# Performance work log

Hardware: AMD Instinct MI355X
Metric: run time of the kernel (lower is better)

Reference implementation:

```python
import jax, jax.numpy as jnp
import numpy as np

C = 256        # channels per FPN level (in_channels == representation_size)
PATCH = 5      # GNN kernel_size == stride
NEG_SLOPE = 0.2
K = 7          # node_connectivities[0]


def _conv1x1(x, w, b):
    return jnp.einsum('bchw,oc->bohw', x, w) + b[None, :, None, None]


def _conv3x3(x, w, b):
    y = jax.lax.conv_general_dilated(x, w, (1, 1), 'SAME',
                                     dimension_numbers=('NCHW', 'OIHW', 'NCHW'))
    return y + b[None, :, None, None]


def _nearest(x, hout, wout):
    hin, win = x.shape[-2:]
    ih = (jnp.arange(hout) * hin) // hout
    iw = (jnp.arange(wout) * win) // wout
    return x[..., ih, :][..., iw]


def _topk_edges(score, k, n):
    # torch: A.scatter(1, topk_idx, topk_val); edge = nonzero(triu(A)); edge=[col,row]
    vals, idx = jax.lax.top_k(score, k)          # per-row top-k
    row = jnp.repeat(jnp.arange(n), k)
    col = idx.reshape(-1)
    val = vals.reshape(-1)
    # triu keeps col>=row; GATv2Conv removes self loops then re-adds one per node
    mask = (col > row) & (val != 0.0)
    loop = jnp.arange(n)
    src = jnp.concatenate([col, loop])           # PyG edge_index[0] = source
    dst = jnp.concatenate([row, loop])
    emask = jnp.concatenate([mask, jnp.ones((n,), bool)])
    return src, dst, emask


def _gatv2(x, src, dst, emask, wl, bl, wr, br, att, bias, n):
    heads, dout = att.shape
    xl = (x @ wl + bl).reshape(n, heads, dout)   # source transform (lin_l)
    xr = (x @ wr + br).reshape(n, heads, dout)   # target transform (lin_r)
    m = xl[src] + xr[dst]                        # [E, H, D]
    e = jnp.sum(jax.nn.leaky_relu(m, NEG_SLOPE) * att[None], axis=-1)  # [E, H]
    e = jnp.where(emask[:, None], e, -1e30)
    emax = jax.ops.segment_max(e, dst, num_segments=n)
    w = jnp.exp(e - emax[dst]) * emask[:, None]
    denom = jax.ops.segment_sum(w, dst, num_segments=n)
    alpha = w / (denom[dst] + 1e-16)
    out = jax.ops.segment_sum(alpha[..., None] * xl[src], dst, num_segments=n)
    return out.reshape(n, heads * dout) + bias


def _gnn(x, p, k):
    # x: [1, C, H, W], H,W divisible by PATCH
    _, c, hh, ww = x.shape
    nh, nw = hh // PATCH, ww // PATCH
    n = nh * nw
    patches = x[0].reshape(c, nh, PATCH, nw, PATCH).transpose(1, 3, 0, 2, 4)
    patches = patches.reshape(n, c, PATCH, PATCH)
    emb = jax.nn.relu(jnp.einsum('ncij,ocij->no', patches, p['conv1_w']) + p['conv1_b'])
    emb = jax.nn.relu(emb @ p['fc2_w'].T + p['fc2_b'])
    # feature-similarity kNN graph
    src, dst, em = _topk_edges(emb @ emb.T, k, n)
    h = jax.nn.elu(_gatv2(emb, src, dst, em, *p['g1'], n))
    h = jax.nn.elu(_gatv2(h, src, dst, em, *p['g2'], n))
    # spatial kNN graph (k smallest distances; self distance 0 drops out via val!=0)
    ii, jj = jnp.meshgrid(jnp.arange(nh) * PATCH, jnp.arange(nw) * PATCH, indexing='ij')
    centers = jnp.stack([ii.reshape(-1), jj.reshape(-1)], -1).astype(x.dtype)
    dist = jnp.sqrt(jnp.sum((centers[:, None] - centers[None]) ** 2, -1))
    src2, dst2, em2 = _topk_edges(-dist, k, n)
    h2 = jax.nn.elu(_gatv2(emb, src2, dst2, em2, *p['g3'], n))
    h2 = jax.nn.elu(_gatv2(h2, src2, dst2, em2, *p['g4'], n))
    hc = jax.nn.relu(jnp.concatenate([h, h2], 1) @ p['fc3_w'].T + p['fc3_b']) + h2
    # torch: reshape(dim,dim,C).swapdims(-1,0) -> [C, nw, nh]
    grid = jnp.transpose(hc.reshape(nh, nw, c), (2, 1, 0))
    # ConvTranspose2d(C, C, 5, stride=5): non-overlapping tiling
    up = jnp.einsum('cij,coab->oiajb', grid, p['convT_w'])
    up = up.reshape(c, nw * PATCH, nh * PATCH) + p['convT_b'][:, None, None]
    return jax.nn.relu(up)[None]


def _forward(feat0, feat1, inner_w, inner_b, layer_w, layer_b, convT_w, convT_b,
             conv1_w, conv1_b, fc2_w, fc2_b, fc3_w, fc3_b,
             g1_wl, g1_bl, g1_wr, g1_br, g1_att, g1_bias,
             g2_wl, g2_bl, g2_wr, g2_br, g2_att, g2_bias,
             g3_wl, g3_bl, g3_wr, g3_br, g3_att, g3_bias,
             g4_wl, g4_bl, g4_wr, g4_br, g4_att, g4_bias, k):
    feats = [feat0, feat1]
    xs = []
    for i, f in enumerate(feats):
        p = dict(conv1_w=conv1_w[i], conv1_b=conv1_b[i],
                 fc2_w=fc2_w[i], fc2_b=fc2_b[i],
                 fc3_w=fc3_w[i], fc3_b=fc3_b[i],
                 convT_w=convT_w[i], convT_b=convT_b[i],
                 g1=(g1_wl[i], g1_bl[i], g1_wr[i], g1_br[i], g1_att[i], g1_bias[i]),
                 g2=(g2_wl[i], g2_bl[i], g2_wr[i], g2_br[i], g2_att[i], g2_bias[i]),
                 g3=(g3_wl[i], g3_bl[i], g3_wr[i], g3_br[i], g3_att[i], g3_bias[i]),
                 g4=(g4_wl[i], g4_bl[i], g4_wr[i], g4_br[i], g4_att[i], g4_bias[i]))
        xs.append(f + _gnn(f, p, k))
    # top-down FPN
    last = _conv1x1(xs[1], inner_w[1], inner_b[1])
    out1 = _conv3x3(last, layer_w[1], layer_b[1])
    inner0 = _conv1x1(xs[0], inner_w[0], inner_b[0])
    td = _nearest(last, xs[0].shape[-2], xs[0].shape[-1])
    out0 = _conv3x3(inner0 + td, layer_w[0], layer_b[0])
    return out0, out1


def setup_inputs() -> dict:
    key = jax.random.key(0)
    keys = jax.random.split(key, 48)
    it = iter(range(48))
    def rn(shape, s=0.05):
        return (jax.random.normal(keys[next(it)], shape) * s).astype(jnp.float32)
    H8 = 8 * C
    inp = dict(
        feat0=rn((1, C, 200, 200), 1.0),
        feat1=rn((1, C, 100, 100), 1.0),
        inner_w=rn((2, C, C)), inner_b=rn((2, C)),
        layer_w=rn((2, C, C, 3, 3)), layer_b=rn((2, C)),
        convT_w=rn((2, C, C, PATCH, PATCH)), convT_b=rn((2, C)),
        conv1_w=rn((2, C, C, PATCH, PATCH)), conv1_b=rn((2, C)),
        fc2_w=rn((2, C, C)), fc2_b=rn((2, C)),
        fc3_w=rn((2, C, 2 * C)), fc3_b=rn((2, C)),
        g1_wl=rn((2, C, H8)), g1_bl=rn((2, H8)), g1_wr=rn((2, C, H8)), g1_br=rn((2, H8)),
        g1_att=rn((2, 8, C)), g1_bias=rn((2, H8)),
        g2_wl=rn((2, H8, C)), g2_bl=rn((2, C)), g2_wr=rn((2, H8, C)), g2_br=rn((2, C)),
        g2_att=rn((2, 1, C)), g2_bias=rn((2, C)),
        g3_wl=rn((2, C, H8)), g3_bl=rn((2, H8)), g3_wr=rn((2, C, H8)), g3_br=rn((2, H8)),
        g3_att=rn((2, 8, C)), g3_bias=rn((2, H8)),
        g4_wl=rn((2, H8, C)), g4_bl=rn((2, C)), g4_wr=rn((2, H8, C)), g4_br=rn((2, C)),
        g4_att=rn((2, 1, C)), g4_bias=rn((2, C)),
        k=K,
    )
    return inp


def reference(feat0, feat1, inner_w, inner_b, layer_w, layer_b, convT_w, convT_b,
              conv1_w, conv1_b, fc2_w, fc2_b, fc3_w, fc3_b,
              g1_wl, g1_bl, g1_wr, g1_br, g1_att, g1_bias,
              g2_wl, g2_bl, g2_wr, g2_br, g2_att, g2_bias,
              g3_wl, g3_bl, g3_wr, g3_br, g3_att, g3_bias,
              g4_wl, g4_bl, g4_wr, g4_br, g4_att, g4_bias, k):
    return _forward(feat0, feat1, inner_w, inner_b, layer_w, layer_b, convT_w, convT_b,
                    conv1_w, conv1_b, fc2_w, fc2_b, fc3_w, fc3_b,
                    g1_wl, g1_bl, g1_wr, g1_br, g1_att, g1_bias,
                    g2_wl, g2_bl, g2_wr, g2_br, g2_att, g2_bias,
                    g3_wl, g3_bl, g3_wr, g3_br, g3_att, g3_bias,
                    g4_wl, g4_bl, g4_wr, g4_br, g4_att, g4_bias, k)
```

## Files before the change

### kernel.cpp

```cpp
#include <hip/hip_runtime.h>
#include <cstdint>
#include <cstddef>
#include <math.h>

#define KNN 7

using short8  = __attribute__((ext_vector_type(8))) short;
using floatx4 = __attribute__((ext_vector_type(4))) float;

static const size_t OFF_ARENA = 0;
static const size_t OFF_XS0   = 10240000;
static const size_t OFF_XS1   = 20480000;
static const size_t OFF_LAST  = 23040000;
static const size_t OFF_EMB   = 25600000;
static const size_t OFF_EMB2  = 26009600;
static const size_t OFF_XL    = 26419200;
static const size_t OFF_H1    = 32972800;
static const size_t OFF_XL2   = 36249600;
static const size_t OFF_CAT   = 37068800;
static const size_t OFF_HC    = 37888000;
static const size_t OFF_SRCF  = 38400000;
static const size_t OFF_SRCS  = 38411200;
static const size_t OFF_BF_A  = 38422400;
static const size_t OFF_BF_W  = 40122400;
// ... 77 lines not shown
            if (ACT == 1) v = fmaxf(v, 0.f);
            C[(size_t)mm * N + nc] = v;
        }
    }
}

template<int ACT, bool BIAS>
static inline void gemm32(hipStream_t s, const float* A, const float* B, const float* bias,
                          float* C, int M, int N, int K)
{
    dim3 g((N + 63) / 64, (M + 63) / 64);
    gemm_k<ACT, BIAS><<<g, dim3(256), 0, s>>>(A, B, bias, C, M, N, K);
}

enum { BT_NT = 0, BT_CONV2 = 2 };

template<int BT, int ACT, int BAX, bool ADDMAT>
__global__ __launch_bounds__(256)
void bgemm_k(const unsigned short* __restrict__ A, const unsigned short* __restrict__ B,
             const float* __restrict__ bias, const float* __restrict__ bias2, int nsplit,
             const float* __restrict__ Dmat, int Dld,
             float* __restrict__ C, int M, int N, int K, int imH, int imW)
{
    __shared__ unsigned short As[3][4096];
    __shared__ unsigned short Bs[3][4096];
    const int tid  = threadIdx.x;
    const int lane = tid & 63;
    const int wid  = tid >> 6;
    const int quad = lane >> 4;
    const int l15  = lane & 15;
    const int wy = wid >> 1, wx = wid & 1;

    int bxx = blockIdx.x, byy = blockIdx.y;
    if (gridDim.y == 2) {
        const int nbx = gridDim.x;
        const int nwg = nbx * 2;
        const int hw  = byy * nbx + bxx;
        const int q = nwg >> 3, r = nwg & 7;
        const int x8 = hw & 7, d = hw >> 3;
        const int lg = (x8 < r) ? x8 * (q + 1) + d : r * (q + 1) + (x8 - r) * q + d;
        byy = lg & 1; bxx = lg >> 1;
    }
    const int bm0 = byy * 128;
    const int bn0 = bxx * 128;

    floatx4 zero = {0.f, 0.f, 0.f, 0.f};
    floatx4 acc[4][4];
    #pragma unroll
    for (int i = 0; i < 4; i++)
        #pragma unroll
        for (int j = 0; j < 4; j++) acc[i][j] = zero;

    const int l4 = lane >> 2;
    const int swc = (((lane & 3) ^ ((lane >> 3) & 3)) << 3);
    const int r0 = wid * 32 + l4;
    const int r1 = r0 + 16;
    int am0 = bm0 + r0; if (am0 > M - 1) am0 = M - 1;
    int am1 = bm0 + r1; if (am1 > M - 1) am1 = M - 1;
    const unsigned short* aP0 = A + (size_t)am0 * K + swc;
    const unsigned short* aP1 = A + (size_t)am1 * K + swc;

    const unsigned short* bP0;
    const unsigned short* bP1;
    if (BT == BT_NT) {
        int bn0r = bn0 + r0; if (bn0r > N - 1) bn0r = N - 1;
        int bn1r = bn0 + r1; if (bn1r > N - 1) bn1r = N - 1;
        bP0 = B + (size_t)bn0r * K + swc;
        bP1 = B + (size_t)bn1r * K + swc;
    } else {
        const int W2 = imW + 2;
        int pp0 = bn0 + r0; if (pp0 > N - 1) pp0 = N - 1;
        int pp1 = bn0 + r1; if (pp1 > N - 1) pp1 = N - 1;
        const int py0 = pp0 / imW, px0 = pp0 - py0 * imW;
        const int py1 = pp1 / imW, px1 = pp1 - py1 * imW;
        bP0 = B + ((size_t)(py0 + 1) * W2 + px0 + 1) * 256 + swc;
        bP1 = B + ((size_t)(py1 + 1) * W2 + px1 + 1) * 256 + swc;
    }

    auto stage = [&](int buf, int t) {
        const int k0 = t << 5;
        glds16(aP0 + k0, &As[buf][wid * 1024]);
        glds16(aP1 + k0, &As[buf][wid * 1024 + 512]);
        if (BT == BT_NT) {
            glds16(bP0 + k0, &Bs[buf][wid * 1024]);
            glds16(bP1 + k0, &Bs[buf][wid * 1024 + 512]);
        } else {
            const int jj = k0 >> 8;
            const int j3 = jj / 3;
            const ptrdiff_t toff = (ptrdiff_t)((j3 - 1) * (imW + 2) + (jj - j3 * 3 - 1)) * 256
                                 + (k0 & 255);
            glds16(bP0 + toff, &Bs[buf][wid * 1024]);
            glds16(bP1 + toff, &Bs[buf][wid * 1024 + 512]);
        }
    };
    const int rsw = ((quad ^ ((l15 >> 1) & 3)) << 3);
    auto compute = [&](int buf) {
        short8 af[4], bfr[4];
        #pragma unroll
        for (int i = 0; i < 4; i++)
            af[i] = *(const short8*)&As[buf][(wy * 64 + i * 16 + l15) * 32 + rsw];
        #pragma unroll
        for (int j = 0; j < 4; j++)
            bfr[j] = *(const short8*)&Bs[buf][(wx * 64 + j * 16 + l15) * 32 + rsw];
        #pragma unroll
        for (int i = 0; i < 4; i++)
            #pragma unroll
            for (int j = 0; j < 4; j++)
                acc[i][j] = __builtin_amdgcn_mfma_f32_16x16x32_bf16(af[i], bfr[j], acc[i][j], 0, 0, 0);
    };

    const int T = K >> 5;
    stage(0, 0);
    if (T > 1) stage(1, 1);
    int cb = 0, sb = 2;
    for (int t = 0; t < T; t++) {
        if (t < T - 1) asm volatile("s_waitcnt vmcnt(4) lgkmcnt(0)" ::: "memory");
        else           asm volatile("s_waitcnt vmcnt(0) lgkmcnt(0)" ::: "memory");
        __builtin_amdgcn_s_barrier();
        __builtin_amdgcn_sched_barrier(0);
        if (t + 2 < T) stage(sb, t + 2);
        compute(cb);
        cb = (cb == 2) ? 0 : cb + 1;
        sb = (sb == 2) ? 0 : sb + 1;
    }

    #pragma unroll
    for (int i = 0; i < 4; i++) {
        #pragma unroll
        for (int r = 0; r < 4; r++) {
            const int m = bm0 + wy * 64 + i * 16 + quad * 4 + r;
            if (m >= M) continue;
            #pragma unroll
            for (int j = 0; j < 4; j++) {
                const int n = bn0 + wx * 64 + j * 16 + l15;
                if (n >= N) continue;
                float v = acc[i][j][r];
                if (bias != nullptr)
                    v += (BAX == 0) ? bias[m] : (n < nsplit ? bias[n] : bias2[n - nsplit]);
                if (ACT == 1) v = fmaxf(v, 0.f);
                if (ADDMAT) v += Dmat[(size_t)m * Dld + n];
                C[(size_t)m * N + n] = v;
            }
        }
    }
}

template<int BT, int ACT, int BAX, bool ADDMAT>
static inline void bgemm(hipStream_t s, const unsigned short* A, const unsigned short* B,
                         const float* bias, const float* bias2, int nsplit,
                         const float* D, int Dld, float* C,
                         int M, int N, int K, int imH = 0, int imW = 0)
{
    dim3 g((N + 127) / 128, (M + 127) / 128);
    bgemm_k<BT, ACT, BAX, ADDMAT><<<g, dim3(256), 0, s>>>(A, B, bias, bias2, nsplit,
                                                          D, Dld, C, M, N, K, imH, imW);
}

__global__ __launch_bounds__(256)
void bgemm_sk_k(const unsigned short* __restrict__ A, const unsigned short* __restrict__ B,
                float* __restrict__ part, int M, int N, int K, int Kc)
{
    __shared__ unsigned short As[3][4096];
    __shared__ unsigned short Bs[3][4096];
    const int tid  = threadIdx.x;
    const int lane = tid & 63;
    const int wid  = tid >> 6;
    const int quad = lane >> 4;
    const int l15  = lane & 15;
    const int wy = wid >> 1, wx = wid & 1;
    const int bm0 = blockIdx.y * 128;
    const int bn0 = blockIdx.x * 128;
    const int kbeg = blockIdx.z * Kc;
    const int kend = (kbeg + Kc < K) ? kbeg + Kc : K;

    floatx4 zero = {0.f, 0.f, 0.f, 0.f};
    floatx4 acc[4][4];
    #pragma unroll
    for (int i = 0; i < 4; i++)
        #pragma unroll
        for (int j = 0; j < 4; j++) acc[i][j] = zero;

    const int l4 = lane >> 2;
    const int swc = (((lane & 3) ^ ((lane >> 3) & 3)) << 3);
    const int r0 = wid * 32 + l4;
    const int r1 = r0 + 16;
    int am0 = bm0 + r0; if (am0 > M - 1) am0 = M - 1;
    int am1 = bm0 + r1; if (am1 > M - 1) am1 = M - 1;
    int bn0r = bn0 + r0; if (bn0r > N - 1) bn0r = N - 1;
    int bn1r = bn0 + r1; if (bn1r > N - 1) bn1r = N - 1;
    const unsigned short* aP0 = A + (size_t)am0 * K + kbeg + swc;
    const unsigned short* aP1 = A + (size_t)am1 * K + kbeg + swc;
    const unsigned short* bP0 = B + (size_t)bn0r * K + kbeg + swc;
    const unsigned short* bP1 = B + (size_t)bn1r * K + kbeg + swc;

    auto stage = [&](int buf, int t) {
        const int k0 = t << 5;
        glds16(aP0 + k0, &As[buf][wid * 1024]);
        glds16(aP1 + k0, &As[buf][wid * 1024 + 512]);
        glds16(bP0 + k0, &Bs[buf][wid * 1024]);
        glds16(bP1 + k0, &Bs[buf][wid * 1024 + 512]);
    };
    const int rsw = ((quad ^ ((l15 >> 1) & 3)) << 3);
    auto compute = [&](int buf) {
        short8 af[4], bfr[4];
        #pragma unroll
        for (int i = 0; i < 4; i++)
            af[i] = *(const short8*)&As[buf][(wy * 64 + i * 16 + l15) * 32 + rsw];
        #pragma unroll
        for (int j = 0; j < 4; j++)
            bfr[j] = *(const short8*)&Bs[buf][(wx * 64 + j * 16 + l15) * 32 + rsw];
        #pragma unroll
        for (int i = 0; i < 4; i++)
            #pragma unroll
            for (int j = 0; j < 4; j++)
                acc[i][j] = __builtin_amdgcn_mfma_f32_16x16x32_bf16(af[i], bfr[j], acc[i][j], 0, 0, 0);
    };

    const int T = (kend - kbeg) >> 5;
    stage(0, 0);
    if (T > 1) stage(1, 1);
    int cb = 0, sb = 2;
    for (int t = 0; t < T; t++) {
        if (t < T - 1) asm volatile("s_waitcnt vmcnt(4) lgkmcnt(0)" ::: "memory");
        else           asm volatile("s_waitcnt vmcnt(0) lgkmcnt(0)" ::: "memory");
        __builtin_amdgcn_s_barrier();
        __builtin_amdgcn_sched_barrier(0);
        if (t + 2 < T) stage(sb, t + 2);
        compute(cb);
        cb = (cb == 2) ? 0 : cb + 1;
        sb = (sb == 2) ? 0 : sb + 1;
    }

    float* P = part + (size_t)blockIdx.z * M * N;
    #pragma unroll
    for (int i = 0; i < 4; i++) {
        #pragma unroll
        for (int r = 0; r < 4; r++) {
            const int m = bm0 + wy * 64 + i * 16 + quad * 4 + r;
            if (m >= M) continue;
            #pragma unroll
            for (int j = 0; j < 4; j++) {
                const int n = bn0 + wx * 64 + j * 16 + l15;
                if (n >= N) continue;
                P[(size_t)m * N + n] = acc[i][j][r];
            }
        }
    }
}

__global__ __launch_bounds__(256)
void bgemm_hilo_sk_k(const unsigned short* __restrict__ Ahi, const unsigned short* __restrict__ Alo,
                     const unsigned short* __restrict__ Bhi, const unsigned short* __restrict__ Blo,
                     float* __restrict__ part, int M, int N, int K, int Kc, int S3)
{
    __shared__ unsigned short As[3][4096];
    __shared__ unsigned short Bs[3][4096];
    const int tid  = threadIdx.x;
    const int lane = tid & 63;
    const int wid  = tid >> 6;
    const int quad = lane >> 4;
    const int l15  = lane & 15;
    const int wy = wid >> 1, wx = wid & 1;
    const int bm0 = blockIdx.y * 128;
    const int bn0 = blockIdx.x * 128;

    const int seg  = blockIdx.z / S3;
    const int slab = blockIdx.z - seg * S3;
    const unsigned short* A = (seg == 1) ? Alo : Ahi;
    const unsigned short* B = (seg == 2) ? Blo : Bhi;
    const int kbeg = slab * Kc;
    const int kend = (kbeg + Kc < K) ? kbeg + Kc : K;

    floatx4 zero = {0.f, 0.f, 0.f, 0.f};
    floatx4 acc[4][4];
    #pragma unroll
    for (int i = 0; i < 4; i++)
        #pragma unroll
        for (int j = 0; j < 4; j++) acc[i][j] = zero;

    const int l4 = lane >> 2;
    const int swc = (((lane & 3) ^ ((lane >> 3) & 3)) << 3);
    const int r0 = wid * 32 + l4;
    const int r1 = r0 + 16;
    int am0 = bm0 + r0; if (am0 > M - 1) am0 = M - 1;
    int am1 = bm0 + r1; if (am1 > M - 1) am1 = M - 1;
    int bn0r = bn0 + r0; if (bn0r > N - 1) bn0r = N - 1;
    int bn1r = bn0 + r1; if (bn1r > N - 1) bn1r = N - 1;
    const unsigned short* aP0 = A + (size_t)am0 * K + kbeg + swc;
    const unsigned short* aP1 = A + (size_t)am1 * K + kbeg + swc;
    const unsigned short* bP0 = B + (size_t)bn0r * K + kbeg + swc;
    const unsigned short* bP1 = B + (size_t)bn1r * K + kbeg + swc;

    auto stage = [&](int buf, int t) {
        const int k0 = t << 5;
        glds16(aP0 + k0, &As[buf][wid * 1024]);
        glds16(aP1 + k0, &As[buf][wid * 1024 + 512]);
        glds16(bP0 + k0, &Bs[buf][wid * 1024]);
        glds16(bP1 + k0, &Bs[buf][wid * 1024 + 512]);
    };
    const int rsw = ((quad ^ ((l15 >> 1) & 3)) << 3);
    auto compute = [&](int buf) {
        short8 af[4], bfr[4];
        #pragma unroll
        for (int i = 0; i < 4; i++)
            af[i] = *(const short8*)&As[buf][(wy * 64 + i * 16 + l15) * 32 + rsw];
        #pragma unroll
        for (int j = 0; j < 4; j++)
            bfr[j] = *(const short8*)&Bs[buf][(wx * 64 + j * 16 + l15) * 32 + rsw];
        #pragma unroll
        for (int i = 0; i < 4; i++)
            #pragma unroll
            for (int j = 0; j < 4; j++)
                acc[i][j] = __builtin_amdgcn_mfma_f32_16x16x32_bf16(af[i], bfr[j], acc[i][j], 0, 0, 0);
    };

    const int T = (kend - kbeg) >> 5;
    stage(0, 0);
    if (T > 1) stage(1, 1);
    int cb = 0, sb = 2;
    for (int t = 0; t < T; t++) {
        if (t < T - 1) asm volatile("s_waitcnt vmcnt(4) lgkmcnt(0)" ::: "memory");
        else           asm volatile("s_waitcnt vmcnt(0) lgkmcnt(0)" ::: "memory");
        __builtin_amdgcn_s_barrier();
        __builtin_amdgcn_sched_barrier(0);
        if (t + 2 < T) stage(sb, t + 2);
        compute(cb);
        cb = (cb == 2) ? 0 : cb + 1;
        sb = (sb == 2) ? 0 : sb + 1;
    }

    float* P = part + (size_t)blockIdx.z * M * N;
    #pragma unroll
    for (int i = 0; i < 4; i++) {
        #pragma unroll
        for (int r = 0; r < 4; r++) {
            const int m = bm0 + wy * 64 + i * 16 + quad * 4 + r;
            if (m >= M) continue;
            #pragma unroll
            for (int j = 0; j < 4; j++) {
                const int n = bn0 + wx * 64 + j * 16 + l15;
                if (n >= N) continue;
                P[(size_t)m * N + n] = acc[i][j][r];
            }
        }
    }
}

template<int ACT, bool ADDMAT>
__global__ void bsk_reduce_k(const float* __restrict__ part,
                             const float* __restrict__ bias, const float* __restrict__ bias2,
                             int nsplit, const float* __restrict__ Dmat, int Dld,
// ... 7 lines not shown
        a.x += b.x; a.y += b.y; a.z += b.z; a.w += b.w;
    }
    const int n = i4 % N;
    const float* bb = (n < nsplit) ? (bias + n) : (bias2 + n - nsplit);
    a.x += bb[0]; a.y += bb[1]; a.z += bb[2]; a.w += bb[3];
    if (ACT == 1) {
        a.x = fmaxf(a.x, 0.f); a.y = fmaxf(a.y, 0.f);
        a.z = fmaxf(a.z, 0.f); a.w = fmaxf(a.w, 0.f);
    }
    if (ADDMAT) {
        const int m = i4 / N;
        const float4 d = *(const float4*)(Dmat + (size_t)m * Dld + n);
        a.x += d.x; a.y += d.y; a.z += d.z; a.w += d.w;
    }
    *(float4*)(C + i4) = a;
}

template<int ACT, bool ADDMAT>
static inline void bgemm_sk(hipStream_t s, const unsigned short* A, const unsigned short* B,
                            const float* bias, const float* bias2, int nsplit,
                            const float* D, int Dld, float* C, float* part,
                            int M, int N, int K, int S)
{
    const int Kc = ((K / S + 31) / 32) * 32;
    dim3 g((N + 127) / 128, (M + 127) / 128, S);
    bgemm_sk_k<<<g, dim3(256), 0, s>>>(A, B, part, M, N, K, Kc);
    const int MN = M * N;
    bsk_reduce_k<ACT, ADDMAT><<<dim3((MN / 4 + 255) / 256), dim3(256), 0, s>>>(
        part, bias, bias2, nsplit, D, Dld, C, MN, N, S);
}

__global__ void cast_bf16_k(const float* __restrict__ in, unsigned short* __restrict__ out, int total)
{
    const int i4 = (blockIdx.x * 256 + threadIdx.x) * 4;
    if (i4 + 4 <= total) {
        const float4 v = *(const float4*)(in + i4);
        ushort4 o;
        o.x = f2bf(v.x); o.y = f2bf(v.y); o.z = f2bf(v.z); o.w = f2bf(v.w);
        *(ushort4*)(out + i4) = o;
    } else {
        for (int i = i4; i < total; i++) out[i] = f2bf(in[i]);
    }
}

static inline void cast_bf(hipStream_t s, const float* in, unsigned short* out, int total)
{
    cast_bf16_k<<<dim3((total / 4 + 255) / 256), dim3(256), 0, s>>>(in, out, total);
// ... 61 lines not shown
{
    cast_t_body(in, out, K, N);
}

__global__ void cast_t2_k(const float* __restrict__ in0, const float* __restrict__ in1,
                          unsigned short* __restrict__ out0, unsigned short* __restrict__ out1,
                          int K, int N)
{
    if (blockIdx.z == 0) cast_t_body(in0, out0, K, N);
    else                 cast_t_body(in1, out1, K, N);
}

static inline void cast_t(hipStream_t s, const float* in, unsigned short* out, int K, int N)
{
    cast_t_k<<<dim3((N + 63) / 64, (K + 63) / 64), dim3(256), 0, s>>>(in, out, K, N);
}

static inline void cast_t2(hipStream_t s, const float* in0, const float* in1,
                           unsigned short* out0, unsigned short* out1, int K, int N)
{
    cast_t2_k<<<dim3((N + 63) / 64, (K + 63) / 64, 2), dim3(256), 0, s>>>(in0, in1, out0, out1, K, N);
}

__global__ void cast_t_pad_k(const float* __restrict__ in, unsigned short* __restrict__ out,
                             int N, int imW)
{
    __shared__ float tile[64][65];
    const int n0 = blockIdx.x * 64;
    const int k0 = blockIdx.y * 64;
    const int t = threadIdx.x;
    const int r = t >> 2;
    const int c4 = (t & 3) << 4;
    {
        const int k = k0 + r;
        if (n0 + c4 + 16 <= N) {
            const float4* p = (const float4*)(in + (size_t)k * N + n0 + c4);
            *(float4*)&tile[r][c4]      = p[0];
            *(float4*)&tile[r][c4 + 4]  = p[1];
            *(float4*)&tile[r][c4 + 8]  = p[2];
            *(float4*)&tile[r][c4 + 12] = p[3];
        } else {
            for (int i = 0; i < 16; i++)
                tile[r][c4 + i] = (n0 + c4 + i < N) ? in[(size_t)k * N + n0 + c4 + i] : 0.f;
        }
    }
    __syncthreads();
    const int n = n0 + r;
    if (n >= N) return;
    const int py = n / imW, px = n - py * imW;
    unsigned short tmp[16];
    #pragma unroll
    for (int i = 0; i < 16; i++) tmp[i] = f2bf(tile[c4 + i][r]);
    unsigned short* o = out + ((size_t)(py + 1) * (imW + 2) + px + 1) * 256 + k0 + c4;
    *(uint4*)(o)     = *(uint4*)&tmp[0];
    *(uint4*)(o + 8) = *(uint4*)&tmp[8];
}

static inline void cast_t_pad(hipStream_t s, const float* in, unsigned short* out, int N, int imW)
{
    cast_t_pad_k<<<dim3((N + 63) / 64, 4), dim3(256), 0, s>>>(in, out, N, imW);
}

__global__ void zero_ring_k(unsigned short* __restrict__ out, int imH, int imW)
{
    const int W2 = imW + 2;
    const int nb = 2 * W2 + 2 * imH;
    const int idx = blockIdx.x * 256 + threadIdx.x;
    if (idx >= nb * 32) return;
    const int p = idx >> 5;
    const int c8 = (idx & 31) << 3;
    int row;
    if (p < W2)            row = p;
    else if (p < 2 * W2)   row = (imH + 1) * W2 + (p - W2);
    else { const int q = p - 2 * W2; const int y = q >> 1;
           row = (y + 1) * W2 + ((q & 1) ? (imW + 1) : 0); }
    *(uint4*)(out + (size_t)row * 256 + c8) = (uint4){0, 0, 0, 0};
}

static inline void zero_ring(hipStream_t s, unsigned short* out, int imH, int imW)
{
    const int tot = (2 * (imW + 2) + 2 * imH) * 32;
    zero_ring_k<<<dim3((tot + 255) / 256), dim3(256), 0, s>>>(out, imH, imW);
}
// ... 167 lines not shown
    o1 = (o1 > 0.f) ? o1 : (expf(o1) - 1.f);
    o2 = (o2 > 0.f) ? o2 : (expf(o2) - 1.f);
    o3 = (o3 > 0.f) ? o3 : (expf(o3) - 1.f);
    float4 res = {o0, o1, o2, o3};
    *(float4*)(out + (size_t)r * ostride + ooff + (size_t)h * 256 + d0) = res;
}

__global__ void scatter_convT_k(const float* __restrict__ f, const float* __restrict__ U,
                                const float* __restrict__ bias, float* __restrict__ xs,
                                int nw, int H, int total)
{
    int idx = blockIdx.x * 256 + threadIdx.x;
    if (idx >= total) return;
    int x = idx % H;
    int t = idx / H;
    int y = t % H;
    int o = t / H;
    int j = y / 5, a = y - j * 5;
    int i = x / 5, b = x - i * 5;
    int p = i * nw + j;
    float v = U[(size_t)p * 6400 + o * 25 + a * 5 + b] + bias[o];
    v = fmaxf(v, 0.f);
    xs[idx] = f[idx] + v;
}

__global__ void upsample_add_k(float* __restrict__ acc, const float* __restrict__ last,
                               int H, int Hs, int total)
{
    int idx = blockIdx.x * 256 + threadIdx.x;
    if (idx >= total) return;
    int x = idx % H;
    int t = idx / H;
    int y = t % H;
    int c = t / H;
    acc[idx] += last[(size_t)c * Hs * Hs + (size_t)(y >> 1) * Hs + (x >> 1)];
}

static void run_level(void* const* d_in, float* ws, int l, int H, hipStream_t s)
{
    const float* f = (const float*)d_in[l];
    const int nh = H / 5, nw = nh, n = nh * nw, HW = H * H;

    const float* convT_w = (const float*)d_in[6]  + (size_t)l * 1638400;
    const float* convT_b = (const float*)d_in[7]  + l * 256;
    const float* conv1_w = (const float*)d_in[8]  + (size_t)l * 1638400;
    const float* conv1_b = (const float*)d_in[9]  + l * 256;
    const float* fc2_w   = (const float*)d_in[10] + (size_t)l * 65536;
    const float* fc2_b   = (const float*)d_in[11] + l * 256;
    const float* fc3_w   = (const float*)d_in[12] + (size_t)l * 131072;
    const float* fc3_b   = (const float*)d_in[13] + l * 256;
    const float* g1_wl   = (const float*)d_in[14] + (size_t)l * 524288;
    const float* g1_bl   = (const float*)d_in[15] + l * 2048;
    const float* g1_wr   = (const float*)d_in[16] + (size_t)l * 524288;
    const float* g1_br   = (const float*)d_in[17] + l * 2048;
    const float* g1_att  = (const float*)d_in[18] + l * 2048;
    const float* g1_bias = (const float*)d_in[19] + l * 2048;
    const float* g2_wl   = (const float*)d_in[20] + (size_t)l * 524288;
    const float* g2_bl   = (const float*)d_in[21] + l * 256;
// ... 8 lines not shown
    const float* g3_att  = (const float*)d_in[30] + l * 2048;
    const float* g3_bias = (const float*)d_in[31] + l * 2048;
    const float* g4_wl   = (const float*)d_in[32] + (size_t)l * 524288;
    const float* g4_bl   = (const float*)d_in[33] + l * 256;
    const float* g4_wr   = (const float*)d_in[34] + (size_t)l * 524288;
    const float* g4_br   = (const float*)d_in[35] + l * 256;
    const float* g4_att  = (const float*)d_in[36] + l * 256;
    const float* g4_bias = (const float*)d_in[37] + l * 256;

    float* patches = ws + OFF_ARENA;
    float* xs    = ws + (l == 0 ? OFF_XS0 : OFF_XS1);
    float* emb   = ws + OFF_EMB;
    float* emb2  = ws + OFF_EMB2;
    float* score = ws + OFF_LAST;
    float* xlr   = ws + OFF_XL;
    float* h1    = ws + OFF_H1;
    float* xlr2  = ws + OFF_XL2;
    float* cat   = ws + OFF_CAT;
    float* hc    = ws + OFF_HC;
    int* srcF = (int*)(ws + OFF_SRCF);
    int* srcS = (int*)(ws + OFF_SRCS);
    unsigned short* ba = (unsigned short*)(ws + OFF_BF_A);
    unsigned short* bw = (unsigned short*)(ws + OFF_BF_W);
    float* part = ws + OFF_ARENA;

    unsigned short* Ahi = (unsigned short*)(ws + OFF_ARENA);
    unsigned short* Alo = Ahi + (size_t)n * 6400;
    unsigned short* Whi = (unsigned short*)(ws + OFF_BF_A);
    unsigned short* Wlo = Whi + 1638400;
    { int tot = n * 6400;
      extract_patches_hilo_k<<<dim3((tot + 255) / 256), dim3(256), 0, s>>>(f, Ahi, Alo, nw, H, tot); }
    cast_hilo_k<<<dim3((1638400 / 4 + 255) / 256), dim3(256), 0, s>>>(conv1_w, Whi, Wlo, 1638400);
    const int S3 = (l == 0) ? 4 : 8;
    { dim3 g(2, (n + 127) / 128, 3 * S3);
      bgemm_hilo_sk_k<<<g, dim3(256), 0, s>>>(Ahi, Alo, Whi, Wlo, xlr, n, 256, 6400, 6400 / S3, S3); }
    { const int MN = n * 256;
      bsk_reduce_k<1, false><<<dim3((MN / 4 + 255) / 256), dim3(256), 0, s>>>(
          xlr, conv1_b, conv1_b, 256, nullptr, 0, emb, MN, 256, 3 * S3); }

    gemm32<1, true>(s, emb, fc2_w, fc2_b, emb2, n, 256, 256);
    gemm32<0, false>(s, emb2, emb2, nullptr, score, n, n, 256);
    topk_feat_k<<<dim3(n), dim3(64), 0, s>>>(score, srcF, n);
    topk_spatial_k<<<dim3(n), dim3(64), 0, s>>>(srcS, n, nw);

    const int gatw1 = n * 8;
    const int gatw2 = n;

    cast_bf(s, emb2, ba, n * 256);
    cast_t2(s, g1_wl, g1_wr, bw, bw + 2048 * 256, 256, 2048);
    if (n >= 1024)
        bgemm<BT_NT, 0, 1, false>(s, ba, bw, g1_bl, g1_br, 2048, nullptr, 0, xlr, n, 4096, 256);
    else
        bgemm_sk<0, false>(s, ba, bw, g1_bl, g1_br, 2048, nullptr, 0, xlr, part, n, 4096, 256, 2);
    gat_fused_k<<<dim3((gatw1 + 3) / 4), dim3(256), 0, s>>>(xlr, 2048, 4096, g1_att, srcF, g1_bias, h1, n, 8, 2048, 0);

    cast_bf(s, h1, ba, n * 2048);
    cast_t2(s, g2_wl, g2_wr, bw, bw + 256 * 2048, 2048, 256);
    bgemm_sk<0, false>(s, ba, bw, g2_bl, g2_br, 256, nullptr, 0, xlr2, part, n, 512, 2048, 8);
    gat_fused_k<<<dim3((gatw2 + 3) / 4), dim3(256), 0, s>>>(xlr2, 256, 512, g2_att, srcF, g2_bias, cat, n, 1, 512, 0);

    cast_bf(s, emb2, ba, n * 256);
    cast_t2(s, g3_wl, g3_wr, bw, bw + 2048 * 256, 256, 2048);
    if (n >= 1024)
        bgemm<BT_NT, 0, 1, false>(s, ba, bw, g3_bl, g3_br, 2048, nullptr, 0, xlr, n, 4096, 256);
    else
        bgemm_sk<0, false>(s, ba, bw, g3_bl, g3_br, 2048, nullptr, 0, xlr, part, n, 4096, 256, 2);
    gat_fused_k<<<dim3((gatw1 + 3) / 4), dim3(256), 0, s>>>(xlr, 2048, 4096, g3_att, srcS, g3_bias, h1, n, 8, 2048, 0);

    cast_bf(s, h1, ba, n * 2048);
    cast_t2(s, g4_wl, g4_wr, bw, bw + 256 * 2048, 2048, 256);
    bgemm_sk<0, false>(s, ba, bw, g4_bl, g4_br, 256, nullptr, 0, xlr2, part, n, 512, 2048, 8);
    gat_fused_k<<<dim3((gatw2 + 3) / 4), dim3(256), 0, s>>>(xlr2, 256, 512, g4_att, srcS, g4_bias, cat, n, 1, 512, 256);

    cast_bf(s, cat, ba, n * 512);
    cast_bf(s, fc3_w, bw, 131072);
    bgemm_sk<1, true>(s, ba, bw, fc3_b, fc3_b, 256, cat + 256, 512, hc, part, n, 256, 512, 4);
    cast_bf(s, hc, ba, n * 256);
    cast_t(s, convT_w, bw, 256, 6400);
    bgemm<BT_NT, 0, 1, false>(s, ba, bw, nullptr, nullptr, 0, nullptr, 0, patches, n, 6400, 256);
    { int tot = 256 * HW;
      scatter_convT_k<<<dim3((tot + 255) / 256), dim3(256), 0, s>>>(f, patches, convT_b, xs, nw, H, tot); }
}

extern "C" void kernel_launch(void* const* d_in, const int* in_sizes, int n_in,
                              void* d_out, int out_size, void* d_ws, size_t ws_size,
                              hipStream_t stream)
{
    float* ws  = (float*)d_ws;
    float* out = (float*)d_out;

    run_level(d_in, ws, 0, 200, stream);
    run_level(d_in, ws, 1, 100, stream);

    const float* inner_w = (const float*)d_in[2];
    const float* inner_b = (const float*)d_in[3];
    const float* layer_w = (const float*)d_in[4];
    const float* layer_b = (const float*)d_in[5];
    float* xs0    = ws + OFF_XS0;
    float* xs1    = ws + OFF_XS1;
    float* last   = ws + OFF_LAST;
    float* inner0 = ws + OFF_ARENA;
    unsigned short* bimg = (unsigned short*)(ws + OFF_XL);
    unsigned short* bw1  = (unsigned short*)(ws + OFF_BF_W);
    unsigned short* bwc  = (unsigned short*)(ws + OFF_BF_W + 100000);

    cast_t(stream, xs1, bimg, 256, 10000);
    cast_bf(stream, inner_w + 65536, bw1, 65536);
    bgemm<BT_NT, 0, 0, false>(stream, bw1, bimg, inner_b + 256, nullptr, 0, nullptr, 0,
                              last, 256, 10000, 256);
    reorder_w3_k<<<dim3((589824 + 255) / 256), dim3(256), 0, stream>>>(layer_w + 589824, bwc);
    zero_ring(stream, bimg, 100, 100);
    cast_t_pad(stream, last, bimg, 10000, 100);
    bgemm<BT_CONV2, 0, 0, false>(stream, bwc, bimg, layer_b + 256, nullptr, 0, nullptr, 0,
                                 out + 10240000, 256, 10000, 2304, 100, 100);

    cast_t(stream, xs0, bimg, 256, 40000);
    cast_bf(stream, inner_w, bw1, 65536);
    bgemm<BT_NT, 0, 0, false>(stream, bw1, bimg, inner_b, nullptr, 0, nullptr, 0,
                              inner0, 256, 40000, 256);
    { int tot = 256 * 40000;
      upsample_add_k<<<dim3((tot + 255) / 256), dim3(256), 0, stream>>>(inner0, last, 200, 100, tot); }
    reorder_w3_k<<<dim3((589824 + 255) / 256), dim3(256), 0, stream>>>(layer_w, bwc);
    zero_ring(stream, bimg, 200, 200);
    cast_t_pad(stream, inner0, bimg, 40000, 200);
    bgemm<BT_CONV2, 0, 0, false>(stream, bwc, bimg, layer_b, nullptr, 0, nullptr, 0,
                                 out, 256, 40000, 2304, 200, 200);
}
```

Measured before the change: 1.116 ms.

## Widen GEMM K-tile to 64 with double buffering and fuse upsample-add into cast

All bf16 MFMA GEMM kernels now stage 64-wide K slices into two LDS buffers with an 8-way XOR swizzle, replacing 32-wide slices in a triple buffer. The loop gains a second barrier per iteration, so fewer iterations and barriers cover the same K, at the cost of less prefetch depth. Split-K chunk sizes are rounded to multiples of 64 to match, including the hilo conv GEMM. The separate upsample-add kernel is folded into the padded transpose-cast of the FPN inner output, and the emb2 bf16 cast is done once and reused by two GAT layers.

After: 1.102 ms. No clear change (-1.2%).

```diff
diff --git a/kernel.cpp b/kernel.cpp
--- a/kernel.cpp
+++ b/kernel.cpp
@@ -123,13 +123,14 @@
              const float* __restrict__ Dmat, int Dld,
              float* __restrict__ C, int M, int N, int K, int imH, int imW)
 {
-    __shared__ unsigned short As[3][4096];
-    __shared__ unsigned short Bs[3][4096];
+    __shared__ unsigned short As[2][8192];
+    __shared__ unsigned short Bs[2][8192];
     const int tid  = threadIdx.x;
     const int lane = tid & 63;
     const int wid  = tid >> 6;
     const int quad = lane >> 4;
     const int l15  = lane & 15;
+    const int l8   = lane >> 3;
     const int wy = wid >> 1, wx = wid & 1;
 
     int bxx = blockIdx.x, byy = blockIdx.y;
@@ -152,77 +153,85 @@
         #pragma unroll
         for (int j = 0; j < 4; j++) acc[i][j] = zero;
 
-    const int l4 = lane >> 2;
-    const int swc = (((lane & 3) ^ ((lane >> 3) & 3)) << 3);
-    const int r0 = wid * 32 + l4;
-    const int r1 = r0 + 16;
-    int am0 = bm0 + r0; if (am0 > M - 1) am0 = M - 1;
-    int am1 = bm0 + r1; if (am1 > M - 1) am1 = M - 1;
-    const unsigned short* aP0 = A + (size_t)am0 * K + swc;
-    const unsigned short* aP1 = A + (size_t)am1 * K + swc;
-
-    const unsigned short* bP0;
-    const unsigned short* bP1;
+    const int swq = (((lane & 7) ^ (l8 & 7)) << 3);
+
+    const unsigned short* aP[4];
+    #pragma unroll
+    for (int g = 0; g < 4; g++) {
+        int r = bm0 + wid * 32 + g * 8 + l8;
+        if (r > M - 1) r = M - 1;
+        aP[g] = A + (size_t)r * K + swq;
+    }
+    const unsigned short* bP[4];
     if (BT == BT_NT) {
-        int bn0r = bn0 + r0; if (bn0r > N - 1) bn0r = N - 1;
-        int bn1r = bn0 + r1; if (bn1r > N - 1) bn1r = N - 1;
-        bP0 = B + (size_t)bn0r * K + swc;
-        bP1 = B + (size_t)bn1r * K + swc;
+        #pragma unroll
+        for (int g = 0; g < 4; g++) {
+            int r = bn0 + wid * 32 + g * 8 + l8;
+            if (r > N - 1) r = N - 1;
+            bP[g] = B + (size_t)r * K + swq;
+        }
     } else {
         const int W2 = imW + 2;
-        int pp0 = bn0 + r0; if (pp0 > N - 1) pp0 = N - 1;
-        int pp1 = bn0 + r1; if (pp1 > N - 1) pp1 = N - 1;
-        const int py0 = pp0 / imW, px0 = pp0 - py0 * imW;
-        const int py1 = pp1 / imW, px1 = pp1 - py1 * imW;
-        bP0 = B + ((size_t)(py0 + 1) * W2 + px0 + 1) * 256 + swc;
-        bP1 = B + ((size_t)(py1 + 1) * W2 + px1 + 1) * 256 + swc;
+        #pragma unroll
+        for (int g = 0; g < 4; g++) {
+            int p = bn0 + wid * 32 + g * 8 + l8;
+            if (p > N - 1) p = N - 1;
+            const int py = p / imW, px = p - py * imW;
+            bP[g] = B + ((size_t)(py + 1) * W2 + px + 1) * 256 + swq;
+        }
     }
 
     auto stage = [&](int buf, int t) {
-        const int k0 = t << 5;
-        glds16(aP0 + k0, &As[buf][wid * 1024]);
-        glds16(aP1 + k0, &As[buf][wid * 1024 + 512]);
+        const int k0 = t << 6;
+        #pragma unroll
+        for (int g = 0; g < 4; g++)
+            glds16(aP[g] + k0, &As[buf][wid * 2048 + g * 512]);
         if (BT == BT_NT) {
-            glds16(bP0 + k0, &Bs[buf][wid * 1024]);
-            glds16(bP1 + k0, &Bs[buf][wid * 1024 + 512]);
+            #pragma unroll
+            for (int g = 0; g < 4; g++)
+                glds16(bP[g] + k0, &Bs[buf][wid * 2048 + g * 512]);
         } else {
             const int jj = k0 >> 8;
             const int j3 = jj / 3;
             const ptrdiff_t toff = (ptrdiff_t)((j3 - 1) * (imW + 2) + (jj - j3 * 3 - 1)) * 256
                                  + (k0 & 255);
-            glds16(bP0 + toff, &Bs[buf][wid * 1024]);
-            glds16(bP1 + toff, &Bs[buf][wid * 1024 + 512]);
+            #pragma unroll
+            for (int g = 0; g < 4; g++)
+                glds16(bP[g] + toff, &Bs[buf][wid * 2048 + g * 512]);
         }
     };
-    const int rsw = ((quad ^ ((l15 >> 1) & 3)) << 3);
     auto compute = [&](int buf) {
-        short8 af[4], bfr[4];
-        #pragma unroll
-        for (int i = 0; i < 4; i++)
-            af[i] = *(const short8*)&As[buf][(wy * 64 + i * 16 + l15) * 32 + rsw];
-        #pragma unroll
-        for (int j = 0; j < 4; j++)
-            bfr[j] = *(const short8*)&Bs[buf][(wx * 64 + j * 16 + l15) * 32 + rsw];
-        #pragma unroll
-        for (int i = 0; i < 4; i++)
+        #pragma unroll
+        for (int ks = 0; ks < 2; ks++) {
+            short8 af[4], bfr[4];
+            #pragma unroll
+            for (int i = 0; i < 4; i++)
+                af[i] = *(const short8*)&As[buf][(wy * 64 + i * 16 + l15) * 64
+                                                 + (((ks * 4 + quad) ^ (l15 & 7)) << 3)];
             #pragma unroll
             for (int j = 0; j < 4; j++)
-                acc[i][j] = __builtin_amdgcn_mfma_f32_16x16x32_bf16(af[i], bfr[j], acc[i][j], 0, 0, 0);
+                bfr[j] = *(const short8*)&Bs[buf][(wx * 64 + j * 16 + l15) * 64
+                                                  + (((ks * 4 + quad) ^ (l15 & 7)) << 3)];
+            #pragma unroll
+            for (int i = 0; i < 4; i++)
+                #pragma unroll
+                for (int j = 0; j < 4; j++)
+                    acc[i][j] = __builtin_amdgcn_mfma_f32_16x16x32_bf16(af[i], bfr[j], acc[i][j], 0, 0, 0);
+        }
     };
 
-    const int T = K >> 5;
+    const int T2 = K >> 6;
     stage(0, 0);
-    if (T > 1) stage(1, 1);
-    int cb = 0, sb = 2;
-    for (int t = 0; t < T; t++) {
-        if (t < T - 1) asm volatile("s_waitcnt vmcnt(4) lgkmcnt(0)" ::: "memory");
-        else           asm volatile("s_waitcnt vmcnt(0) lgkmcnt(0)" ::: "memory");
+    if (T2 > 1) stage(1, 1);
+    for (int t = 0; t < T2; t++) {
+        if (t + 1 < T2) asm volatile("s_waitcnt vmcnt(8) lgkmcnt(0)" ::: "memory");
+        else            asm volatile("s_waitcnt vmcnt(0) lgkmcnt(0)" ::: "memory");
         __builtin_amdgcn_s_barrier();
         __builtin_amdgcn_sched_barrier(0);
-        if (t + 2 < T) stage(sb, t + 2);
-        compute(cb);
-        cb = (cb == 2) ? 0 : cb + 1;
-        sb = (sb == 2) ? 0 : sb + 1;
+        compute(t & 1);
+        __builtin_amdgcn_s_barrier();
+        __builtin_amdgcn_sched_barrier(0);
+        if (t + 2 < T2) stage(t & 1, t + 2);
     }
 
     #pragma unroll
@@ -261,13 +270,14 @@
 void bgemm_sk_k(const unsigned short* __restrict__ A, const unsigned short* __restrict__ B,
                 float* __restrict__ part, int M, int N, int K, int Kc)
 {
-    __shared__ unsigned short As[3][4096];
-    __shared__ unsigned short Bs[3][4096];
+    __shared__ unsigned short As[2][8192];
+    __shared__ unsigned short Bs[2][8192];
     const int tid  = threadIdx.x;
     const int lane = tid & 63;
     const int wid  = tid >> 6;
     const int quad = lane >> 4;
     const int l15  = lane & 15;
+    const int l8   = lane >> 3;
     const int wy = wid >> 1, wx = wid & 1;
     const int bm0 = blockIdx.y * 128;
     const int bn0 = blockIdx.x * 128;
@@ -281,55 +291,60 @@
         #pragma unroll
         for (int j = 0; j < 4; j++) acc[i][j] = zero;
 
-    const int l4 = lane >> 2;
-    const int swc = (((lane & 3) ^ ((lane >> 3) & 3)) << 3);
-    const int r0 = wid * 32 + l4;
-    const int r1 = r0 + 16;
-    int am0 = bm0 + r0; if (am0 > M - 1) am0 = M - 1;
-    int am1 = bm0 + r1; if (am1 > M - 1) am1 = M - 1;
-    int bn0r = bn0 + r0; if (bn0r > N - 1) bn0r = N - 1;
-    int bn1r = bn0 + r1; if (bn1r > N - 1) bn1r = N - 1;
-    const unsigned short* aP0 = A + (size_t)am0 * K + kbeg + swc;
-    const unsigned short* aP1 = A + (size_t)am1 * K + kbeg + swc;
-    const unsigned short* bP0 = B + (size_t)bn0r * K + kbeg + swc;
-    const unsigned short* bP1 = B + (size_t)bn1r * K + kbeg + swc;
+    const int swq = (((lane & 7) ^ (l8 & 7)) << 3);
+    const unsigned short* aP[4];
+    const unsigned short* bP[4];
+    #pragma unroll
+    for (int g = 0; g < 4; g++) {
+        int ra = bm0 + wid * 32 + g * 8 + l8;
+        if (ra > M - 1) ra = M - 1;
+        aP[g] = A + (size_t)ra * K + kbeg + swq;
+        int rb = bn0 + wid * 32 + g * 8 + l8;
+        if (rb > N - 1) rb = N - 1;
+        bP[g] = B + (size_t)rb * K + kbeg + swq;
+    }
 
     auto stage = [&](int buf, int t) {
-        const int k0 = t << 5;
-        glds16(aP0 + k0, &As[buf][wid * 1024]);
-        glds16(aP1 + k0, &As[buf][wid * 1024 + 512]);
-        glds16(bP0 + k0, &Bs[buf][wid * 1024]);
-        glds16(bP1 + k0, &Bs[buf][wid * 1024 + 512]);
+        const int k0 = t << 6;
+        #pragma unroll
+        for (int g = 0; g < 4; g++)
+            glds16(aP[g] + k0, &As[buf][wid * 2048 + g * 512]);
+        #pragma unroll
+        for (int g = 0; g < 4; g++)
+            glds16(bP[g] + k0, &Bs[buf][wid * 2048 + g * 512]);
     };
-    const int rsw = ((quad ^ ((l15 >> 1) & 3)) << 3);
     auto compute = [&](int buf) {
-        short8 af[4], bfr[4];
-        #pragma unroll
-        for (int i = 0; i < 4; i++)
-            af[i] = *(const short8*)&As[buf][(wy * 64 + i * 16 + l15) * 32 + rsw];
-        #pragma unroll
-        for (int j = 0; j < 4; j++)
-            bfr[j] = *(const short8*)&Bs[buf][(wx * 64 + j * 16 + l15) * 32 + rsw];
-        #pragma unroll
-        for (int i = 0; i < 4; i++)
+        #pragma unroll
+        for (int ks = 0; ks < 2; ks++) {
+            short8 af[4], bfr[4];
+            #pragma unroll
+            for (int i = 0; i < 4; i++)
+                af[i] = *(const short8*)&As[buf][(wy * 64 + i * 16 + l15) * 64
+                                                 + (((ks * 4 + quad) ^ (l15 & 7)) << 3)];
             #pragma unroll
             for (int j = 0; j < 4; j++)
-                acc[i][j] = __builtin_amdgcn_mfma_f32_16x16x32_bf16(af[i], bfr[j], acc[i][j], 0, 0, 0);
+                bfr[j] = *(const short8*)&Bs[buf][(wx * 64 + j * 16 + l15) * 64
+                                                  + (((ks * 4 + quad) ^ (l15 & 7)) << 3)];
+            #pragma unroll
+            for (int i = 0; i < 4; i++)
+                #pragma unroll
+                for (int j = 0; j < 4; j++)
+                    acc[i][j] = __builtin_amdgcn_mfma_f32_16x16x32_bf16(af[i], bfr[j], acc[i][j], 0, 0, 0);
+        }
     };
 
-    const int T = (kend - kbeg) >> 5;
+    const int T2 = (kend - kbeg) >> 6;
     stage(0, 0);
-    if (T > 1) stage(1, 1);
-    int cb = 0, sb = 2;
-    for (int t = 0; t < T; t++) {
-        if (t < T - 1) asm volatile("s_waitcnt vmcnt(4) lgkmcnt(0)" ::: "memory");
-        else           asm volatile("s_waitcnt vmcnt(0) lgkmcnt(0)" ::: "memory");
+    if (T2 > 1) stage(1, 1);
+    for (int t = 0; t < T2; t++) {
+        if (t + 1 < T2) asm volatile("s_waitcnt vmcnt(8) lgkmcnt(0)" ::: "memory");
+        else            asm volatile("s_waitcnt vmcnt(0) lgkmcnt(0)" ::: "memory");
         __builtin_amdgcn_s_barrier();
         __builtin_amdgcn_sched_barrier(0);
-        if (t + 2 < T) stage(sb, t + 2);
-        compute(cb);
-        cb = (cb == 2) ? 0 : cb + 1;
-        sb = (sb == 2) ? 0 : sb + 1;
+        compute(t & 1);
+        __builtin_amdgcn_s_barrier();
+        __builtin_amdgcn_sched_barrier(0);
+        if (t + 2 < T2) stage(t & 1, t + 2);
     }
 
     float* P = part + (size_t)blockIdx.z * M * N;
@@ -354,13 +369,14 @@
                      const unsigned short* __restrict__ Bhi, const unsigned short* __restrict__ Blo,
                      float* __restrict__ part, int M, int N, int K, int Kc, int S3)
 {
-    __shared__ unsigned short As[3][4096];
-    __shared__ unsigned short Bs[3][4096];
+    __shared__ unsigned short As[2][8192];
+    __shared__ unsigned short Bs[2][8192];
     const int tid  = threadIdx.x;
     const int lane = tid & 63;
     const int wid  = tid >> 6;
     const int quad = lane >> 4;
     const int l15  = lane & 15;
+    const int l8   = lane >> 3;
     const int wy = wid >> 1, wx = wid & 1;
     const int bm0 = blockIdx.y * 128;
     const int bn0 = blockIdx.x * 128;
@@ -379,55 +395,60 @@
         #pragma unroll
         for (int j = 0; j < 4; j++) acc[i][j] = zero;
 
-    const int l4 = lane >> 2;
-    const int swc = (((lane & 3) ^ ((lane >> 3) & 3)) << 3);
-    const int r0 = wid * 32 + l4;
-    const int r1 = r0 + 16;
-    int am0 = bm0 + r0; if (am0 > M - 1) am0 = M - 1;
-    int am1 = bm0 + r1; if (am1 > M - 1) am1 = M - 1;
-    int bn0r = bn0 + r0; if (bn0r > N - 1) bn0r = N - 1;
-    int bn1r = bn0 + r1; if (bn1r > N - 1) bn1r = N - 1;
-    const unsigned short* aP0 = A + (size_t)am0 * K + kbeg + swc;
-    const unsigned short* aP1 = A + (size_t)am1 * K + kbeg + swc;
-    const unsigned short* bP0 = B + (size_t)bn0r * K + kbeg + swc;
-    const unsigned short* bP1 = B + (size_t)bn1r * K + kbeg + swc;
+    const int swq = (((lane & 7) ^ (l8 & 7)) << 3);
+    const unsigned short* aP[4];
+    const unsigned short* bP[4];
+    #pragma unroll
+    for (int g = 0; g < 4; g++) {
+        int ra = bm0 + wid * 32 + g * 8 + l8;
+        if (ra > M - 1) ra = M - 1;
+        aP[g] = A + (size_t)ra * K + kbeg + swq;
+        int rb = bn0 + wid * 32 + g * 8 + l8;
+        if (rb > N - 1) rb = N - 1;
+        bP[g] = B + (size_t)rb * K + kbeg + swq;
+    }
 
     auto stage = [&](int buf, int t) {
-        const int k0 = t << 5;
-        glds16(aP0 + k0, &As[buf][wid * 1024]);
-        glds16(aP1 + k0, &As[buf][wid * 1024 + 512]);
-        glds16(bP0 + k0, &Bs[buf][wid * 1024]);
-        glds16(bP1 + k0, &Bs[buf][wid * 1024 + 512]);
+        const int k0 = t << 6;
+        #pragma unroll
+        for (int g = 0; g < 4; g++)
+            glds16(aP[g] + k0, &As[buf][wid * 2048 + g * 512]);
+        #pragma unroll
+        for (int g = 0; g < 4; g++)
+            glds16(bP[g] + k0, &Bs[buf][wid * 2048 + g * 512]);
     };
-    const int rsw = ((quad ^ ((l15 >> 1) & 3)) << 3);
     auto compute = [&](int buf) {
-        short8 af[4], bfr[4];
-        #pragma unroll
-        for (int i = 0; i < 4; i++)
-            af[i] = *(const short8*)&As[buf][(wy * 64 + i * 16 + l15) * 32 + rsw];
-        #pragma unroll
-        for (int j = 0; j < 4; j++)
-            bfr[j] = *(const short8*)&Bs[buf][(wx * 64 + j * 16 + l15) * 32 + rsw];
-        #pragma unroll
-        for (int i = 0; i < 4; i++)
+        #pragma unroll
+        for (int ks = 0; ks < 2; ks++) {
+            short8 af[4], bfr[4];
+            #pragma unroll
+            for (int i = 0; i < 4; i++)
+                af[i] = *(const short8*)&As[buf][(wy * 64 + i * 16 + l15) * 64
+                                                 + (((ks * 4 + quad) ^ (l15 & 7)) << 3)];
             #pragma unroll
             for (int j = 0; j < 4; j++)
-                acc[i][j] = __builtin_amdgcn_mfma_f32_16x16x32_bf16(af[i], bfr[j], acc[i][j], 0, 0, 0);
+                bfr[j] = *(const short8*)&Bs[buf][(wx * 64 + j * 16 + l15) * 64
+                                                  + (((ks * 4 + quad) ^ (l15 & 7)) << 3)];
+            #pragma unroll
+            for (int i = 0; i < 4; i++)
+                #pragma unroll
+                for (int j = 0; j < 4; j++)
+                    acc[i][j] = __builtin_amdgcn_mfma_f32_16x16x32_bf16(af[i], bfr[j], acc[i][j], 0, 0, 0);
+        }
     };
 
-    const int T = (kend - kbeg) >> 5;
+    const int T2 = (kend - kbeg) >> 6;
     stage(0, 0);
-    if (T > 1) stage(1, 1);
-    int cb = 0, sb = 2;
-    for (int t = 0; t < T; t++) {
-        if (t < T - 1) asm volatile("s_waitcnt vmcnt(4) lgkmcnt(0)" ::: "memory");
-        else           asm volatile("s_waitcnt vmcnt(0) lgkmcnt(0)" ::: "memory");
+    if (T2 > 1) stage(1, 1);
+    for (int t = 0; t < T2; t++) {
+        if (t + 1 < T2) asm volatile("s_waitcnt vmcnt(8) lgkmcnt(0)" ::: "memory");
+        else            asm volatile("s_waitcnt vmcnt(0) lgkmcnt(0)" ::: "memory");
         __builtin_amdgcn_s_barrier();
         __builtin_amdgcn_sched_barrier(0);
-        if (t + 2 < T) stage(sb, t + 2);
-        compute(cb);
-        cb = (cb == 2) ? 0 : cb + 1;
-        sb = (sb == 2) ? 0 : sb + 1;
+        compute(t & 1);
+        __builtin_amdgcn_s_barrier();
+        __builtin_amdgcn_sched_barrier(0);
+        if (t + 2 < T2) stage(t & 1, t + 2);
     }
 
     float* P = part + (size_t)blockIdx.z * M * N;
@@ -481,7 +502,7 @@
                             const float* D, int Dld, float* C, float* part,
                             int M, int N, int K, int S)
 {
-    const int Kc = ((K / S + 31) / 32) * 32;
+    const int Kc = ((K / S + 63) / 64) * 64;
     dim3 g((N + 127) / 128, (M + 127) / 128, S);
     bgemm_sk_k<<<g, dim3(256), 0, s>>>(A, B, part, M, N, K, Kc);
     const int MN = M * N;
@@ -589,8 +610,8 @@
     cast_t2_k<<<dim3((N + 63) / 64, (K + 63) / 64, 2), dim3(256), 0, s>>>(in0, in1, out0, out1, K, N);
 }
 
-__global__ void cast_t_pad_k(const float* __restrict__ in, unsigned short* __restrict__ out,
-                             int N, int imW)
+__global__ void cast_t_pad_k(const float* __restrict__ in, const float* __restrict__ up,
+                             unsigned short* __restrict__ out, int N, int imW, int upW)
 {
     __shared__ float tile[64][65];
     const int n0 = blockIdx.x * 64;
@@ -616,16 +637,24 @@
     if (n >= N) return;
     const int py = n / imW, px = n - py * imW;
     unsigned short tmp[16];
-    #pragma unroll
-    for (int i = 0; i < 16; i++) tmp[i] = f2bf(tile[c4 + i][r]);
+    if (up != nullptr) {
+        const float* u = up + (size_t)(py >> 1) * upW + (px >> 1);
+        #pragma unroll
+        for (int i = 0; i < 16; i++)
+            tmp[i] = f2bf(tile[c4 + i][r] + u[(size_t)(k0 + c4 + i) * upW * upW]);
+    } else {
+        #pragma unroll
+        for (int i = 0; i < 16; i++) tmp[i] = f2bf(tile[c4 + i][r]);
+    }
     unsigned short* o = out + ((size_t)(py + 1) * (imW + 2) + px + 1) * 256 + k0 + c4;
     *(uint4*)(o)     = *(uint4*)&tmp[0];
     *(uint4*)(o + 8) = *(uint4*)&tmp[8];
 }
 
-static inline void cast_t_pad(hipStream_t s, const float* in, unsigned short* out, int N, int imW)
-{
-    cast_t_pad_k<<<dim3((N + 63) / 64, 4), dim3(256), 0, s>>>(in, out, N, imW);
+static inline void cast_t_pad(hipStream_t s, const float* in, const float* up,
+                              unsigned short* out, int N, int imW, int upW)
+{
+    cast_t_pad_k<<<dim3((N + 63) / 64, 4), dim3(256), 0, s>>>(in, up, out, N, imW, upW);
 }
 
 __global__ void zero_ring_k(unsigned short* __restrict__ out, int imH, int imW)
@@ -839,18 +868,6 @@
     float v = U[(size_t)p * 6400 + o * 25 + a * 5 + b] + bias[o];
     v = fmaxf(v, 0.f);
     xs[idx] = f[idx] + v;
-}
-
-__global__ void upsample_add_k(float* __restrict__ acc, const float* __restrict__ last,
-                               int H, int Hs, int total)
-{
-    int idx = blockIdx.x * 256 + threadIdx.x;
-    if (idx >= total) return;
-    int x = idx % H;
-    int t = idx / H;
-    int y = t % H;
-    int c = t / H;
-    acc[idx] += last[(size_t)c * Hs * Hs + (size_t)(y >> 1) * Hs + (x >> 1)];
 }
 
 static void run_level(void* const* d_in, float* ws, int l, int H, hipStream_t s)
@@ -905,6 +922,7 @@
     int* srcS = (int*)(ws + OFF_SRCS);
     unsigned short* ba = (unsigned short*)(ws + OFF_BF_A);
     unsigned short* bw = (unsigned short*)(ws + OFF_BF_W);
+    unsigned short* e2b = (unsigned short*)(ws + OFF_EMB);
     float* part = ws + OFF_ARENA;
 
     unsigned short* Ahi = (unsigned short*)(ws + OFF_ARENA);
@@ -915,8 +933,9 @@
       extract_patches_hilo_k<<<dim3((tot + 255) / 256), dim3(256), 0, s>>>(f, Ahi, Alo, nw, H, tot); }
     cast_hilo_k<<<dim3((1638400 / 4 + 255) / 256), dim3(256), 0, s>>>(conv1_w, Whi, Wlo, 1638400);
     const int S3 = (l == 0) ? 4 : 8;
+    const int Kc1 = ((6400 / S3 + 63) / 64) * 64;
     { dim3 g(2, (n + 127) / 128, 3 * S3);
-      bgemm_hilo_sk_k<<<g, dim3(256), 0, s>>>(Ahi, Alo, Whi, Wlo, xlr, n, 256, 6400, 6400 / S3, S3); }
+      bgemm_hilo_sk_k<<<g, dim3(256), 0, s>>>(Ahi, Alo, Whi, Wlo, xlr, n, 256, 6400, Kc1, S3); }
     { const int MN = n * 256;
       bsk_reduce_k<1, false><<<dim3((MN / 4 + 255) / 256), dim3(256), 0, s>>>(
           xlr, conv1_b, conv1_b, 256, nullptr, 0, emb, MN, 256, 3 * S3); }
@@ -929,12 +948,13 @@
     const int gatw1 = n * 8;
     const int gatw2 = n;
 
-    cast_bf(s, emb2, ba, n * 256);
+    cast_bf(s, emb2, e2b, n * 256);
+
     cast_t2(s, g1_wl, g1_wr, bw, bw + 2048 * 256, 256, 2048);
     if (n >= 1024)
-        bgemm<BT_NT, 0, 1, false>(s, ba, bw, g1_bl, g1_br, 2048, nullptr, 0, xlr, n, 4096, 256);
+        bgemm<BT_NT, 0, 1, false>(s, e2b, bw, g1_bl, g1_br, 2048, nullptr, 0, xlr, n, 4096, 256);
     else
-        bgemm_sk<0, false>(s, ba, bw, g1_bl, g1_br, 2048, nullptr, 0, xlr, part, n, 4096, 256, 2);
+        bgemm_sk<0, false>(s, e2b, bw, g1_bl, g1_br, 2048, nullptr, 0, xlr, part, n, 4096, 256, 2);
     gat_fused_k<<<dim3((gatw1 + 3) / 4), dim3(256), 0, s>>>(xlr, 2048, 4096, g1_att, srcF, g1_bias, h1, n, 8, 2048, 0);
 
     cast_bf(s, h1, ba, n * 2048);
@@ -942,12 +962,11 @@
     bgemm_sk<0, false>(s, ba, bw, g2_bl, g2_br, 256, nullptr, 0, xlr2, part, n, 512, 2048, 8);
     gat_fused_k<<<dim3((gatw2 + 3) / 4), dim3(256), 0, s>>>(xlr2, 256, 512, g2_att, srcF, g2_bias, cat, n, 1, 512, 0);
 
-    cast_bf(s, emb2, ba, n * 256);
     cast_t2(s, g3_wl, g3_wr, bw, bw + 2048 * 256, 256, 2048);
     if (n >= 1024)
-        bgemm<BT_NT, 0, 1, false>(s, ba, bw, g3_bl, g3_br, 2048, nullptr, 0, xlr, n, 4096, 256);
+        bgemm<BT_NT, 0, 1, false>(s, e2b, bw, g3_bl, g3_br, 2048, nullptr, 0, xlr, n, 4096, 256);
     else
-        bgemm_sk<0, false>(s, ba, bw, g3_bl, g3_br, 2048, nullptr, 0, xlr, part, n, 4096, 256, 2);
+        bgemm_sk<0, false>(s, e2b, bw, g3_bl, g3_br, 2048, nullptr, 0, xlr, part, n, 4096, 256, 2);
     gat_fused_k<<<dim3((gatw1 + 3) / 4), dim3(256), 0, s>>>(xlr, 2048, 4096, g3_att, srcS, g3_bias, h1, n, 8, 2048, 0);
 
     cast_bf(s, h1, ba, n * 2048);
@@ -993,7 +1012,7 @@
                               last, 256, 10000, 256);
     reorder_w3_k<<<dim3((589824 + 255) / 256), dim3(256), 0, stream>>>(layer_w + 589824, bwc);
     zero_ring(stream, bimg, 100, 100);
-    cast_t_pad(stream, last, bimg, 10000, 100);
+    cast_t_pad(stream, last, nullptr, bimg, 10000, 100, 0);
     bgemm<BT_CONV2, 0, 0, false>(stream, bwc, bimg, layer_b + 256, nullptr, 0, nullptr, 0,
                                  out + 10240000, 256, 10000, 2304, 100, 100);
 
@@ -1001,11 +1020,9 @@
     cast_bf(stream, inner_w, bw1, 65536);
     bgemm<BT_NT, 0, 0, false>(stream, bw1, bimg, inner_b, nullptr, 0, nullptr, 0,
                               inner0, 256, 40000, 256);
-    { int tot = 256 * 40000;
-      upsample_add_k<<<dim3((tot + 255) / 256), dim3(256), 0, stream>>>(inner0, last, 200, 100, tot); }
     reorder_w3_k<<<dim3((589824 + 255) / 256), dim3(256), 0, stream>>>(layer_w, bwc);
     zero_ring(stream, bimg, 200, 200);
-    cast_t_pad(stream, inner0, bimg, 40000, 200);
+    cast_t_pad(stream, inner0, last, bimg, 40000, 200, 100);
     bgemm<BT_CONV2, 0, 0, false>(stream, bwc, bimg, layer_b, nullptr, 0, nullptr, 0,
                                  out, 256, 40000, 2304, 200, 200);
 }
```
